# Kernel tuning notes

Hardware: AMD Instinct MI355X
Metric: run time of the kernel (lower is better)

The kernel has to match this reference:

```python
import jax, jax.numpy as jnp
import numpy as np

D_MODEL = 512
N_HEADS = 8
HEAD_DIM = D_MODEL // N_HEADS
B, L, S = 4, 2048, 2048


def setup_inputs() -> dict:
    key = jax.random.key(0)
    ks = jax.random.split(key, 16)
    std = 1.0 / np.sqrt(D_MODEL)
    inp = {
        'queries': jax.random.normal(ks[0], (B, L, D_MODEL), jnp.float32),
        'keys': jax.random.normal(ks[1], (B, S, D_MODEL), jnp.float32),
        'values': jax.random.normal(ks[2], (B, S, D_MODEL), jnp.float32),
        'tau': jax.random.uniform(ks[3], (B,), jnp.float32, 0.5, 1.5),
        'delta': jax.random.normal(ks[4], (B,), jnp.float32) * 0.1,
        'Wq': jax.random.normal(ks[5], (D_MODEL, D_MODEL), jnp.float32) * std,
        'bq': jnp.zeros((D_MODEL,), jnp.float32),
        'Wk': jax.random.normal(ks[6], (D_MODEL, D_MODEL), jnp.float32) * std,
        'bk': jnp.zeros((D_MODEL,), jnp.float32),
        'Wv': jax.random.normal(ks[7], (D_MODEL, D_MODEL), jnp.float32) * std,
        'bv': jnp.zeros((D_MODEL,), jnp.float32),
        'Wo': jax.random.normal(ks[8], (D_MODEL, D_MODEL), jnp.float32) * std,
        'bo': jnp.zeros((D_MODEL,), jnp.float32),
    }
    return inp


def reference(queries, keys, values, tau, delta, Wq, bq, Wk, bk, Wv, bv, Wo, bo):
    Bq, Lq, _ = queries.shape
    Sk = keys.shape[1]
    H, E = N_HEADS, HEAD_DIM
    # projections -> [B, L, H, E]
    q = (queries @ Wq + bq).reshape(Bq, Lq, H, E)
    k = (keys @ Wk + bk).reshape(Bq, Sk, H, E)
    v = (values @ Wv + bv).reshape(Bq, Sk, H, E)
    scale = 1.0 / jnp.sqrt(jnp.float32(E))
    # scores: [B, H, L, S]
    scores = jnp.einsum('blhe,bshe->bhls', q, k)
    scores = scores * tau[:, None, None, None] + delta[:, None, None, None]
    A = jax.nn.softmax(scale * scores, axis=-1)  # dropout is identity in eval
    out = jnp.einsum('bhls,bshd->blhd', A, v).reshape(Bq, Lq, H * E)
    return out @ Wo + bo
```

## Files before the change

kernel.cpp:

```cpp
#include <hip/hip_runtime.h>
#include <stdint.h>

#define NB 4
#define LQ 2048
#define DM 512
#define NH 8
#define EH 64
#define MT (NB*LQ)
#define QBLK 128

typedef __attribute__((ext_vector_type(4)))  float f32x4;
typedef __attribute__((ext_vector_type(8)))  __bf16 bf16x8;
typedef __attribute__((ext_vector_type(8)))  unsigned short u16x8;
typedef __attribute__((ext_vector_type(4)))  short s16x4;
typedef __attribute__((ext_vector_type(4)))  float float4_t;
typedef __attribute__((ext_vector_type(2)))  unsigned int u32x2;

static __device__ __forceinline__ unsigned short f2bf(float f) {
  unsigned int u = __builtin_bit_cast(unsigned int, f);
  u += 0x7fffu + ((u >> 16) & 1u);
  return (unsigned short)(u >> 16);
}

static __device__ __forceinline__ float bf2f(unsigned short h) {
  unsigned int u = ((unsigned int)h) << 16;
  return __builtin_bit_cast(float, u);
}

static __device__ __forceinline__ void gload16(const void* g, void* l) {
  __builtin_amdgcn_global_load_lds(
      (__attribute__((address_space(1))) unsigned int*)(g),
      (__attribute__((address_space(3))) unsigned int*)(l), 16, 0, 0);
}

static __device__ __forceinline__ unsigned int cvt_pk_bf16(float lo, float hi) {
  unsigned int r;
  asm("v_cvt_pk_bf16_f32 %0, %1, %2" : "=v"(r) : "v"(lo), "v"(hi));
  return r;
}

static __device__ __forceinline__ f32x4 mfma16(s16x4 a, s16x4 b, f32x4 c) {
#if defined(__HIP_DEVICE_COMPILE__)
#if __has_builtin(__builtin_amdgcn_mfma_f32_16x16x16bf16_1k)
  return __builtin_amdgcn_mfma_f32_16x16x16bf16_1k(a, b, c, 0, 0, 0);
#else
  f32x4 d;
  asm volatile("v_mfma_f32_16x16x16_bf16 %0, %1, %2, %3"
               : "=v"(d) : "v"(a), "v"(b), "0"(c));
  return d;
#endif
#else
  (void)a; (void)b;
  return c;
#endif
}

extern "C" __global__ __launch_bounds__(256) void k_cast_x(
    const float* __restrict__ q, const float* __restrict__ k,
    const float* __restrict__ v, unsigned short* __restrict__ x) {
  int z = blockIdx.y;
  const float* src = (z == 0) ? q : ((z == 1) ? k : v);
  unsigned short* dst = x + (size_t)z * MT * DM;
  size_t i = ((size_t)blockIdx.x * 256 + threadIdx.x) * 8;
  float4_t a = *(const float4_t*)(src + i);
  float4_t b = *(const float4_t*)(src + i + 4);
  u16x8 r;
  r[0]=f2bf(a[0]); r[1]=f2bf(a[1]); r[2]=f2bf(a[2]); r[3]=f2bf(a[3]);
  r[4]=f2bf(b[0]); r[5]=f2bf(b[1]); r[6]=f2bf(b[2]); r[7]=f2bf(b[3]);
  *(u16x8*)(dst + i) = r;
}

extern "C" __global__ __launch_bounds__(256) void k_cast_wt(
    const float* __restrict__ wq, const float* __restrict__ wk,
    const float* __restrict__ wv, const float* __restrict__ wo,
    unsigned short* __restrict__ wt) {
  __shared__ float tile[64][65];
  int z = blockIdx.z;
  const float* w = (z==0)?wq : (z==1)?wk : (z==2)?wv : wo;
  unsigned short* dst = wt + (size_t)z * DM * DM;
  int kb = blockIdx.y * 64, nb = blockIdx.x * 64;
  int t = threadIdx.x;
  int r = t >> 2, c0 = (t & 3) * 16;
  #pragma unroll
  for (int i = 0; i < 16; i += 4) {
    float4_t v4 = *(const float4_t*)(w + (size_t)(kb + r) * DM + nb + c0 + i);
    tile[r][c0+i]   = v4[0]; tile[r][c0+i+1] = v4[1];
    tile[r][c0+i+2] = v4[2]; tile[r][c0+i+3] = v4[3];
  }
  __syncthreads();
  u16x8 o0, o1;
  #pragma unroll
  for (int i = 0; i < 8; ++i) o0[i] = f2bf(tile[c0+i][r]);
  #pragma unroll
  for (int i = 0; i < 8; ++i) o1[i] = f2bf(tile[c0+8+i][r]);
  *(u16x8*)(dst + (size_t)(nb + r) * DM + kb + c0)     = o0;
  *(u16x8*)(dst + (size_t)(nb + r) * DM + kb + c0 + 8) = o1;
}

extern "C" __global__ __launch_bounds__(256) void k_gemm_qkv(
    const unsigned short* __restrict__ X, const unsigned short* __restrict__ WT,
    const float* __restrict__ bq, const float* __restrict__ bk,
    const float* __restrict__ bv, const float* __restrict__ tau,
    unsigned short* __restrict__ out) {
  int z = blockIdx.z;
  const unsigned short* A  = X  + (size_t)z * MT * DM;
  const unsigned short* Bt = WT + (size_t)z * DM * DM;
  const float* bias = (z==0)?bq : (z==1)?bk : bv;
  unsigned short* dst = out + (size_t)z * MT * DM;

  __shared__ unsigned short As[2][128][32];
  __shared__ unsigned short Bs[2][128][32];

  int m0 = blockIdx.y * 128;
  int n0 = blockIdx.x * 128;
  float qsc = (z == 0) ? tau[m0 >> 11] * 0.18033688011112042f : 1.0f;
  int t = threadIdx.x;
  int lane = t & 63;
  int w = t >> 6;
  int wr = w >> 1, wc = w & 1;
  int g = lane >> 4, r15 = lane & 15;

  f32x4 acc[4][4];
  #pragma unroll
  for (int i=0;i<4;i++)
    #pragma unroll
    for (int j=0;j<4;j++)
      #pragma unroll
      for (int e=0;e<4;e++) acc[i][j][e] = 0.f;

  auto stage = [&](int bb, int kt) {
    int k0 = kt * 32;
    int sblk = (t & 3) ^ ((t >> 3) & 3);
    #pragma unroll
    for (int j=0;j<2;j++) {
      int o = t*16 + j*4096;
      int row = o >> 6;
      gload16(A  + (size_t)(m0+row)*DM + k0 + sblk*8, (char*)(&As[bb][0][0]) + o);
      gload16(Bt + (size_t)(n0+row)*DM + k0 + sblk*8, (char*)(&Bs[bb][0][0]) + o);
    }
  };

  stage(0, 0);
  __syncthreads();
  int buf = 0;
  for (int kt = 0; kt < DM/32; ++kt) {
    if (kt + 1 < DM/32) stage(buf ^ 1, kt + 1);
    bf16x8 af[4], bfr[4];
    #pragma unroll
    for (int mi=0;mi<4;mi++) {
      int row = wr*64 + mi*16 + r15;
      int blk = g ^ ((row >> 1) & 3);
      af[mi] = *(const bf16x8*)(&As[buf][row][blk*8]);
    }
    #pragma unroll
    for (int ni=0;ni<4;ni++) {
      int row = wc*64 + ni*16 + r15;
      int blk = g ^ ((row >> 1) & 3);
      bfr[ni] = *(const bf16x8*)(&Bs[buf][row][blk*8]);
    }
    #pragma unroll
    for (int mi=0;mi<4;mi++)
      #pragma unroll
      for (int ni=0;ni<4;ni++)
        acc[mi][ni] = __builtin_amdgcn_mfma_f32_16x16x32_bf16(af[mi], bfr[ni], acc[mi][ni], 0, 0, 0);
    __syncthreads();
    buf ^= 1;
  }
  #pragma unroll
  for (int ni=0;ni<4;ni++) {
    int n = n0 + wc*64 + ni*16 + r15;
    float bia = bias[n];
    int h = n >> 6, e = n & 63;
    #pragma unroll
    for (int mi=0;mi<4;mi++) {
      #pragma unroll
      for (int rg=0;rg<4;rg++) {
        int m = m0 + wr*64 + mi*16 + g*4 + rg;
        int b = m >> 11, s = m & 2047;
        dst[((size_t)((b*NH + h)*LQ + s))*EH + e] = f2bf((acc[mi][ni][rg] + bia) * qsc);
      }
    }
  }
}

extern "C" __global__ __launch_bounds__(256) void k_vt(
    const unsigned short* __restrict__ qkv, unsigned short* __restrict__ vtg) {
  __shared__ unsigned short tile[64][65];
  int bh = blockIdx.y;
  int s0 = blockIdx.x * 64;
  const unsigned short* Vh = qkv + (size_t)2*MT*DM + (size_t)bh*LQ*EH;
  unsigned short* Ot = vtg + (size_t)bh*EH*LQ;
  int t = threadIdx.x;
  int r = t >> 2, c0 = (t & 3) * 16;
  u16x8 a = *(const u16x8*)(Vh + (size_t)(s0 + r)*EH + c0);
  u16x8 b = *(const u16x8*)(Vh + (size_t)(s0 + r)*EH + c0 + 8);
  #pragma unroll
  for (int i=0;i<8;i++) { tile[r][c0+i] = a[i]; tile[r][c0+8+i] = b[i]; }
  __syncthreads();
  int gg = t & 3;
  int er = t >> 2;
  int s2 = (er ^ (er >> 3)) & 3;
  #pragma unroll
  for (int blk = 0; blk < 2; ++blk) {
    u16x8 o;
    #pragma unroll
    for (int j = 0; j < 8; ++j) {
      int sp = blk*32 + (j >> 2)*16 + gg*4 + (j & 3);
      o[j] = tile[sp][er];
    }
    *(u16x8*)(Ot + (size_t)er*LQ + s0 + blk*32 + 8*(gg ^ s2)) = o;
  }
}

template<int NSPLIT>
__global__ __launch_bounds__(256, 4) void k_flash(
    const unsigned short* __restrict__ qkv, const unsigned short* __restrict__ vtg,
    unsigned short* __restrict__ aout,
    unsigned short* __restrict__ opart, float* __restrict__ lpart) {
  constexpr int SKV = LQ / NSPLIT;
  constexpr int NIT = SKV / 32;
  constexpr int CPX = (512 * NSPLIT) / 8;
  int bid = blockIdx.x;
  int wgid = (bid & 7) * CPX + (bid >> 3);
  int part = wgid % NSPLIT;
  int rest = wgid / NSPLIT;
  int qblk = rest & 15;
  int bh = rest >> 4;
  int batch = bh >> 3, h = bh & 7;

  const unsigned short* Qh  = qkv + (size_t)bh * LQ * EH + (size_t)qblk * QBLK * EH;
  const unsigned short* Kh  = qkv + (size_t)MT * DM + (size_t)bh * LQ * EH + (size_t)part * SKV * EH;
  const unsigned short* VTh = vtg + (size_t)bh * EH * LQ + (size_t)part * SKV;

  __shared__ unsigned short Ks[2][32][64];
  __shared__ unsigned short Vt[2][64][32];

  int t = threadIdx.x;
  int lane = t & 63;
  int wv = t >> 6;
  int q4 = lane & 15;
  int g  = lane >> 4;

  auto stage = [&](int bb, int it) {
    int o = t * 16;
    int krow = t >> 3;
    int sblk = (t & 7) ^ ((krow ^ (krow >> 3)) & 7);
    gload16(Kh + (size_t)(it*32 + krow)*EH + sblk*8, (char*)(&Ks[bb][0][0]) + o);
    gload16(VTh + (size_t)(t >> 2)*LQ + it*32 + (t & 3)*8, (char*)(&Vt[bb][0][0]) + o);
  };

  bf16x8 qf[2][2];
  #pragma unroll
  for (int qt=0;qt<2;qt++)
    #pragma unroll
    for (int st=0;st<2;st++)
      qf[qt][st] = *(const bf16x8*)(Qh + (size_t)(wv*32 + qt*16 + q4)*EH + st*32 + g*8);

  stage(0, 0);

  const f32x4 Z4 = {0.f, 0.f, 0.f, 0.f};
  f32x4 oacc[4][2];
  #pragma unroll
  for (int a=0;a<4;a++)
    #pragma unroll
    for (int b2=0;b2<2;b2++)
      #pragma unroll
      for (int e=0;e<4;e++) oacc[a][b2][e] = 0.f;
  float lsp[2] = {0.f, 0.f};

  __syncthreads();
  int buf = 0;
  for (int it = 0; it < NIT; ++it) {
    if (it + 1 < NIT) stage(buf ^ 1, it + 1);

    f32x4 sac[2][2];
    __builtin_amdgcn_s_setprio(1);
    #pragma unroll
    for (int kvt=0; kvt<2; ++kvt) {
      int row = kvt*16 + q4;
      int S = (row ^ (row >> 3)) & 7;
      bf16x8 kf0 = *(const bf16x8*)(&Ks[buf][row][(g ^ S)*8]);
      sac[kvt][0] = __builtin_amdgcn_mfma_f32_16x16x32_bf16(kf0, qf[0][0], Z4, 0,0,0);
      sac[kvt][1] = __builtin_amdgcn_mfma_f32_16x16x32_bf16(kf0, qf[1][0], Z4, 0,0,0);
    }
    #pragma unroll
    for (int kvt=0; kvt<2; ++kvt) {
      int row = kvt*16 + q4;
      int S = (row ^ (row >> 3)) & 7;
      bf16x8 kf1 = *(const bf16x8*)(&Ks[buf][row][((4 + g) ^ S)*8]);
      sac[kvt][0] = __builtin_amdgcn_mfma_f32_16x16x32_bf16(kf1, qf[0][1], sac[kvt][0], 0,0,0);
      sac[kvt][1] = __builtin_amdgcn_mfma_f32_16x16x32_bf16(kf1, qf[1][1], sac[kvt][1], 0,0,0);
    }
    __builtin_amdgcn_s_setprio(0);

    s16x4 pk[2][2];
    #pragma unroll
    for (int qt=0; qt<2; ++qt) {
      #pragma unroll
      for (int kvt=0; kvt<2; ++kvt) {
        float p0 = __builtin_amdgcn_exp2f(sac[kvt][qt][0]);
        float p1 = __builtin_amdgcn_exp2f(sac[kvt][qt][1]);
        float p2 = __builtin_amdgcn_exp2f(sac[kvt][qt][2]);
        float p3 = __builtin_amdgcn_exp2f(sac[kvt][qt][3]);
        lsp[qt] += (p0 + p1) + (p2 + p3);
        union { u32x2 u; s16x4 h; } pu;
        pu.u[0] = cvt_pk_bf16(p0, p1);
        pu.u[1] = cvt_pk_bf16(p2, p3);
        pk[qt][kvt] = pu.h;
      }
    }

    __builtin_amdgcn_s_setprio(1);
    #pragma unroll
    for (int et=0; et<4; ++et) {
      int row = et*16 + q4;
      int s2 = (row ^ (row >> 3)) & 3;
      union { u16x8 w; s16x4 h[2]; } vu;
      vu.w = *(const u16x8*)(&Vt[buf][row][(g ^ s2)*8]);
      oacc[et][0] = mfma16(vu.h[0], pk[0][0], oacc[et][0]);
      oacc[et][0] = mfma16(vu.h[1], pk[0][1], oacc[et][0]);
      oacc[et][1] = mfma16(vu.h[0], pk[1][0], oacc[et][1]);
      oacc[et][1] = mfma16(vu.h[1], pk[1][1], oacc[et][1]);
    }
    __builtin_amdgcn_s_setprio(0);

    __syncthreads();
    buf ^= 1;
  }

  #pragma unroll
  for (int qt=0; qt<2; ++qt) {
    float s = lsp[qt];
    s += __shfl_xor(s, 16, 64);
    s += __shfl_xor(s, 32, 64);
    int q = qblk*QBLK + wv*32 + qt*16 + q4;
    if constexpr (NSPLIT == 1) {
      float inv = 1.f / s;
      unsigned short* rowp = aout + (size_t)(batch*LQ + q)*DM + h*EH;
      #pragma unroll
      for (int et=0; et<4; ++et) {
        #pragma unroll
        for (int rg=0; rg<4; rg+=2) {
          int e = et*16 + g*4 + rg;
          *(unsigned int*)(rowp + e) = cvt_pk_bf16(oacc[et][qt][rg] * inv, oacc[et][qt][rg+1] * inv);
        }
      }
    } else {
      size_t r = (size_t)bh * LQ + q;
      unsigned short* od = opart + ((size_t)r*NSPLIT + part) * 64;
      #pragma unroll
      for (int et=0; et<4; ++et) {
        u32x2 wpk;
        wpk[0] = cvt_pk_bf16(oacc[et][qt][0], oacc[et][qt][1]);
        wpk[1] = cvt_pk_bf16(oacc[et][qt][2], oacc[et][qt][3]);
        *(u32x2*)(od + et*16 + g*4) = wpk;
      }
      if (g == 0) lpart[r*NSPLIT + part] = s;
    }
  }
}

extern "C" __global__ __launch_bounds__(256) void k_red(
    const unsigned short* __restrict__ op, const float* __restrict__ lp,
    unsigned short* __restrict__ aout) {
  int t = threadIdx.x;
  int r = blockIdx.x * 16 + (t >> 4);
  int e0 = (t & 15) * 4;
  float acc0 = 0.f, acc1 = 0.f, acc2 = 0.f, acc3 = 0.f, ls = 0.f;
  #pragma unroll
  for (int qq = 0; qq < 4; ++qq) {
    u32x2 wv = *(const u32x2*)(op + ((size_t)r*4 + qq)*64 + e0);
    acc0 += bf2f((unsigned short)(wv[0] & 0xFFFF));
    acc1 += bf2f((unsigned short)(wv[0] >> 16));
    acc2 += bf2f((unsigned short)(wv[1] & 0xFFFF));
    acc3 += bf2f((unsigned short)(wv[1] >> 16));
    ls += lp[(size_t)r*4 + qq];
  }
  float inv = 1.f / ls;
  int bh = r >> 11, q = r & 2047, batch = bh >> 3, h = bh & 7;
  unsigned short* dst = aout + (size_t)(batch*LQ + q)*DM + h*EH + e0;
  u32x2 w;
  w[0] = cvt_pk_bf16(acc0 * inv, acc1 * inv);
  w[1] = cvt_pk_bf16(acc2 * inv, acc3 * inv);
  *(u32x2*)dst = w;
}

extern "C" __global__ __launch_bounds__(256) void k_gemm_out(
    const unsigned short* __restrict__ A, const unsigned short* __restrict__ WT,
    const float* __restrict__ bo, float* __restrict__ out) {
  const unsigned short* Bt = WT + (size_t)3 * DM * DM;

  __shared__ unsigned short As[2][128][32];
  __shared__ unsigned short Bs[2][128][32];

  int m0 = blockIdx.y * 128;
  int n0 = blockIdx.x * 128;
  int t = threadIdx.x;
  int lane = t & 63;
  int w = t >> 6;
  int wr = w >> 1, wc = w & 1;
  int g = lane >> 4, r15 = lane & 15;

  f32x4 acc[4][4];
  #pragma unroll
  for (int i=0;i<4;i++)
    #pragma unroll
    for (int j=0;j<4;j++)
      #pragma unroll
      for (int e=0;e<4;e++) acc[i][j][e] = 0.f;

  auto stage = [&](int bb, int kt) {
    int k0 = kt * 32;
    int sblk = (t & 3) ^ ((t >> 3) & 3);
    #pragma unroll
    for (int j=0;j<2;j++) {
      int o = t*16 + j*4096;
      int row = o >> 6;
      gload16(A  + (size_t)(m0+row)*DM + k0 + sblk*8, (char*)(&As[bb][0][0]) + o);
      gload16(Bt + (size_t)(n0+row)*DM + k0 + sblk*8, (char*)(&Bs[bb][0][0]) + o);
    }
  };

  stage(0, 0);
  __syncthreads();
  int buf = 0;
  for (int kt = 0; kt < DM/32; ++kt) {
    if (kt + 1 < DM/32) stage(buf ^ 1, kt + 1);
    bf16x8 af[4], bfr[4];
    #pragma unroll
    for (int mi=0;mi<4;mi++) {
      int row = wr*64 + mi*16 + r15;
      int blk = g ^ ((row >> 1) & 3);
      af[mi] = *(const bf16x8*)(&As[buf][row][blk*8]);
    }
    #pragma unroll
    for (int ni=0;ni<4;ni++) {
      int row = wc*64 + ni*16 + r15;
      int blk = g ^ ((row >> 1) & 3);
      bfr[ni] = *(const bf16x8*)(&Bs[buf][row][blk*8]);
    }
    #pragma unroll
    for (int mi=0;mi<4;mi++)
      #pragma unroll
      for (int ni=0;ni<4;ni++)
        acc[mi][ni] = __builtin_amdgcn_mfma_f32_16x16x32_bf16(af[mi], bfr[ni], acc[mi][ni], 0, 0, 0);
    __syncthreads();
    buf ^= 1;
  }
  #pragma unroll
  for (int ni=0;ni<4;ni++) {
    int n = n0 + wc*64 + ni*16 + r15;
    float bia = bo[n];
    #pragma unroll
    for (int mi=0;mi<4;mi++) {
      #pragma unroll
      for (int rg=0;rg<4;rg++) {
        int m = m0 + wr*64 + mi*16 + g*4 + rg;
        out[(size_t)m*DM + n] = acc[mi][ni][rg] + bia;
      }
    }
  }
}

extern "C" void kernel_launch(void* const* d_in, const int* in_sizes, int n_in,
                              void* d_out, int out_size, void* d_ws, size_t ws_size,
                              hipStream_t stream) {
  const float* queries = (const float*)d_in[0];
  const float* keys    = (const float*)d_in[1];
  const float* values  = (const float*)d_in[2];
  const float* tau     = (const float*)d_in[3];
  const float* Wq = (const float*)d_in[5];
  const float* bq = (const float*)d_in[6];
  const float* Wk = (const float*)d_in[7];
  const float* bk = (const float*)d_in[8];
  const float* Wv = (const float*)d_in[9];
  const float* bv = (const float*)d_in[10];
  const float* Wo = (const float*)d_in[11];
  const float* bo = (const float*)d_in[12];
  float* out = (float*)d_out;

  char* ws = (char*)d_ws;
  unsigned short* WT   = (unsigned short*)(ws);
  unsigned short* X    = (unsigned short*)(ws + (2u  << 20));
  unsigned short* VTg  = (unsigned short*)(ws + (2u  << 20));
  unsigned short* AOut = (unsigned short*)(ws + (10u << 20));
  unsigned short* QKV  = (unsigned short*)(ws + (26u << 20));
  unsigned short* Opart= (unsigned short*)(ws + (50u << 20));
  float*          Lpart= (float*)(ws + (84u << 20));

  k_cast_x  <<<dim3(2048, 3), dim3(256), 0, stream>>>(queries, keys, values, X);
  k_cast_wt <<<dim3(8, 8, 4), dim3(256), 0, stream>>>(Wq, Wk, Wv, Wo, WT);
  k_gemm_qkv<<<dim3(4, 64, 3), dim3(256), 0, stream>>>(X, WT, bq, bk, bv, tau, QKV);
  k_vt      <<<dim3(32, 32), dim3(256), 0, stream>>>(QKV, VTg);

  if (ws_size >= ((size_t)85u << 20)) {
    k_flash<4><<<dim3(2048), dim3(256), 0, stream>>>(QKV, VTg, AOut, Opart, Lpart);
    k_red    <<<dim3(4096), dim3(256), 0, stream>>>(Opart, Lpart, AOut);
  } else {
    k_flash<1><<<dim3(512), dim3(256), 0, stream>>>(QKV, VTg, AOut, Opart, Lpart);
  }
  k_gemm_out<<<dim3(4, 64), dim3(256), 0, stream>>>(AOut, WT, bo, out);
}
```

Before: 117.4 us.

## Fuse fp32→bf16 input cast into QKV GEMM and triple-buffer flash K/V staging

Removes the separate k_cast_x pass: the QKV GEMM now loads fp32 activations directly into registers, converts them to bf16 and writes them into swizzled LDS, prefetching one k-tile ahead. This avoids writing and re-reading a bf16 copy of all three inputs. The GEMM grid is also flattened to 1D with an XCD-aware block remap. The flash kernel moves from double to triple-buffered K/V LDS with explicit vmcnt waits and raw barriers, keeping two tiles in flight. The costs are more VGPR pressure and conversion work inside the GEMM, more LDS in the flash kernel, and hand-written waitcnt logic that must match the number of outstanding loads.

```diff
diff --git a/kernel.cpp b/kernel.cpp
--- a/kernel.cpp
+++ b/kernel.cpp
@@ -15,6 +15,7 @@
 typedef __attribute__((ext_vector_type(4)))  short s16x4;
 typedef __attribute__((ext_vector_type(4)))  float float4_t;
 typedef __attribute__((ext_vector_type(2)))  unsigned int u32x2;
+typedef __attribute__((ext_vector_type(4)))  unsigned int u32x4;
 
 static __device__ __forceinline__ unsigned short f2bf(float f) {
   unsigned int u = __builtin_bit_cast(unsigned int, f);
@@ -55,21 +56,6 @@
 #endif
 }
 
-extern "C" __global__ __launch_bounds__(256) void k_cast_x(
-    const float* __restrict__ q, const float* __restrict__ k,
-    const float* __restrict__ v, unsigned short* __restrict__ x) {
-  int z = blockIdx.y;
-  const float* src = (z == 0) ? q : ((z == 1) ? k : v);
-  unsigned short* dst = x + (size_t)z * MT * DM;
-  size_t i = ((size_t)blockIdx.x * 256 + threadIdx.x) * 8;
-  float4_t a = *(const float4_t*)(src + i);
-  float4_t b = *(const float4_t*)(src + i + 4);
-  u16x8 r;
-  r[0]=f2bf(a[0]); r[1]=f2bf(a[1]); r[2]=f2bf(a[2]); r[3]=f2bf(a[3]);
-  r[4]=f2bf(b[0]); r[5]=f2bf(b[1]); r[6]=f2bf(b[2]); r[7]=f2bf(b[3]);
-  *(u16x8*)(dst + i) = r;
-}
-
 extern "C" __global__ __launch_bounds__(256) void k_cast_wt(
     const float* __restrict__ wq, const float* __restrict__ wk,
     const float* __restrict__ wv, const float* __restrict__ wo,
@@ -98,12 +84,19 @@
 }
 
 extern "C" __global__ __launch_bounds__(256) void k_gemm_qkv(
-    const unsigned short* __restrict__ X, const unsigned short* __restrict__ WT,
+    const float* __restrict__ qin, const float* __restrict__ kin,
+    const float* __restrict__ vin, const unsigned short* __restrict__ WT,
     const float* __restrict__ bq, const float* __restrict__ bk,
     const float* __restrict__ bv, const float* __restrict__ tau,
     unsigned short* __restrict__ out) {
-  int z = blockIdx.z;
-  const unsigned short* A  = X  + (size_t)z * MT * DM;
+  int bid = blockIdx.x;
+  int wgid = (bid & 7) * 96 + (bid >> 3);
+  int n0 = (wgid & 3) * 128;
+  int p = wgid >> 2;
+  int z = p % 3;
+  int m0 = (p / 3) * 128;
+
+  const float* Af = (z==0)?qin : (z==1)?kin : vin;
   const unsigned short* Bt = WT + (size_t)z * DM * DM;
   const float* bias = (z==0)?bq : (z==1)?bk : bv;
   unsigned short* dst = out + (size_t)z * MT * DM;
@@ -111,8 +104,6 @@
   __shared__ unsigned short As[2][128][32];
   __shared__ unsigned short Bs[2][128][32];
 
-  int m0 = blockIdx.y * 128;
-  int n0 = blockIdx.x * 128;
   float qsc = (z == 0) ? tau[m0 >> 11] * 0.18033688011112042f : 1.0f;
   int t = threadIdx.x;
   int lane = t & 63;
@@ -120,31 +111,55 @@
   int wr = w >> 1, wc = w & 1;
   int g = lane >> 4, r15 = lane & 15;
 
-  f32x4 acc[4][4];
-  #pragma unroll
-  for (int i=0;i<4;i++)
-    #pragma unroll
-    for (int j=0;j<4;j++)
-      #pragma unroll
-      for (int e=0;e<4;e++) acc[i][j][e] = 0.f;
-
-  auto stage = [&](int bb, int kt) {
+  int ar = t >> 1, ah = t & 1;
+  int as = (ar >> 1) & 3;
+  int dlo = ((ah*2)     ^ as) * 8;
+  int dhi = ((ah*2 + 1) ^ as) * 8;
+
+  float4_t a0, a1, a2, a3;
+  auto loadA = [&](int kt) {
+    const float* src = Af + (size_t)(m0 + ar)*DM + kt*32 + ah*16;
+    a0 = *(const float4_t*)(src);
+    a1 = *(const float4_t*)(src + 4);
+    a2 = *(const float4_t*)(src + 8);
+    a3 = *(const float4_t*)(src + 12);
+  };
+  auto writeA = [&](int bb) {
+    u32x4 lo, hi;
+    lo[0] = cvt_pk_bf16(a0[0], a0[1]); lo[1] = cvt_pk_bf16(a0[2], a0[3]);
+    lo[2] = cvt_pk_bf16(a1[0], a1[1]); lo[3] = cvt_pk_bf16(a1[2], a1[3]);
+    hi[0] = cvt_pk_bf16(a2[0], a2[1]); hi[1] = cvt_pk_bf16(a2[2], a2[3]);
+    hi[2] = cvt_pk_bf16(a3[0], a3[1]); hi[3] = cvt_pk_bf16(a3[2], a3[3]);
+    *(u32x4*)(&As[bb][ar][dlo]) = lo;
+    *(u32x4*)(&As[bb][ar][dhi]) = hi;
+  };
+  auto stageB = [&](int bb, int kt) {
     int k0 = kt * 32;
     int sblk = (t & 3) ^ ((t >> 3) & 3);
     #pragma unroll
     for (int j=0;j<2;j++) {
       int o = t*16 + j*4096;
       int row = o >> 6;
-      gload16(A  + (size_t)(m0+row)*DM + k0 + sblk*8, (char*)(&As[bb][0][0]) + o);
       gload16(Bt + (size_t)(n0+row)*DM + k0 + sblk*8, (char*)(&Bs[bb][0][0]) + o);
     }
   };
 
-  stage(0, 0);
+  f32x4 acc[4][4];
+  #pragma unroll
+  for (int i=0;i<4;i++)
+    #pragma unroll
+    for (int j=0;j<4;j++)
+      #pragma unroll
+      for (int e=0;e<4;e++) acc[i][j][e] = 0.f;
+
+  loadA(0);
+  writeA(0);
+  stageB(0, 0);
   __syncthreads();
   int buf = 0;
   for (int kt = 0; kt < DM/32; ++kt) {
-    if (kt + 1 < DM/32) stage(buf ^ 1, kt + 1);
+    bool pre = (kt + 1 < DM/32);
+    if (pre) { loadA(kt + 1); stageB(buf ^ 1, kt + 1); }
     bf16x8 af[4], bfr[4];
     #pragma unroll
     for (int mi=0;mi<4;mi++) {
@@ -163,6 +178,7 @@
       #pragma unroll
       for (int ni=0;ni<4;ni++)
         acc[mi][ni] = __builtin_amdgcn_mfma_f32_16x16x32_bf16(af[mi], bfr[ni], acc[mi][ni], 0, 0, 0);
+    if (pre) writeA(buf ^ 1);
     __syncthreads();
     buf ^= 1;
   }
@@ -232,8 +248,8 @@
   const unsigned short* Kh  = qkv + (size_t)MT * DM + (size_t)bh * LQ * EH + (size_t)part * SKV * EH;
   const unsigned short* VTh = vtg + (size_t)bh * EH * LQ + (size_t)part * SKV;
 
-  __shared__ unsigned short Ks[2][32][64];
-  __shared__ unsigned short Vt[2][64][32];
+  __shared__ unsigned short Ks[3][32][64];
+  __shared__ unsigned short Vt[3][64][32];
 
   int t = threadIdx.x;
   int lane = t & 63;
@@ -256,8 +272,6 @@
     for (int st=0;st<2;st++)
       qf[qt][st] = *(const bf16x8*)(Qh + (size_t)(wv*32 + qt*16 + q4)*EH + st*32 + g*8);
 
-  stage(0, 0);
-
   const f32x4 Z4 = {0.f, 0.f, 0.f, 0.f};
   f32x4 oacc[4][2];
   #pragma unroll
@@ -268,10 +282,18 @@
       for (int e=0;e<4;e++) oacc[a][b2][e] = 0.f;
   float lsp[2] = {0.f, 0.f};
 
-  __syncthreads();
-  int buf = 0;
+  stage(0, 0);
+  if (NIT > 1) stage(1, 1);
+  asm volatile("s_waitcnt vmcnt(0)" ::: "memory");
+  __builtin_amdgcn_s_barrier();
+
   for (int it = 0; it < NIT; ++it) {
-    if (it + 1 < NIT) stage(buf ^ 1, it + 1);
+    int buf = it % 3;
+    __builtin_amdgcn_s_barrier();
+    if (it + 2 < NIT) stage((it + 2) % 3, it + 2);
+    asm volatile("s_waitcnt vmcnt(4)" ::: "memory");
+    __builtin_amdgcn_s_barrier();
+    __builtin_amdgcn_sched_barrier(0);
 
     f32x4 sac[2][2];
     __builtin_amdgcn_s_setprio(1);
@@ -323,9 +345,6 @@
       oacc[et][1] = mfma16(vu.h[1], pk[1][1], oacc[et][1]);
     }
     __builtin_amdgcn_s_setprio(0);
-
-    __syncthreads();
-    buf ^= 1;
   }
 
   #pragma unroll
@@ -481,16 +500,15 @@
 
   char* ws = (char*)d_ws;
   unsigned short* WT   = (unsigned short*)(ws);
-  unsigned short* X    = (unsigned short*)(ws + (2u  << 20));
   unsigned short* VTg  = (unsigned short*)(ws + (2u  << 20));
   unsigned short* AOut = (unsigned short*)(ws + (10u << 20));
   unsigned short* QKV  = (unsigned short*)(ws + (26u << 20));
   unsigned short* Opart= (unsigned short*)(ws + (50u << 20));
   float*          Lpart= (float*)(ws + (84u << 20));
 
-  k_cast_x  <<<dim3(2048, 3), dim3(256), 0, stream>>>(queries, keys, values, X);
   k_cast_wt <<<dim3(8, 8, 4), dim3(256), 0, stream>>>(Wq, Wk, Wv, Wo, WT);
-  k_gemm_qkv<<<dim3(4, 64, 3), dim3(256), 0, stream>>>(X, WT, bq, bk, bv, tau, QKV);
+  k_gemm_qkv<<<dim3(768), dim3(256), 0, stream>>>(queries, keys, values, WT,
+                                                  bq, bk, bv, tau, QKV);
   k_vt      <<<dim3(32, 32), dim3(256), 0, stream>>>(QKV, VTg);
 
   if (ws_size >= ((size_t)85u << 20)) {
```

Result: faster. 108.3 us (-7.7%).
